# Kernel optimization log

Hardware: AMD Instinct MI355X
Metric: run time of the kernel (lower is better)

The kernel has to match this reference:

```python
import jax, jax.numpy as jnp
import numpy as np

H = W = 128          # render resolution
TS = 4               # texture_size from the module
DIST, ELEV, AZIM = 2.732, 0.0, 90.0   # camera (azimuth fixed for determinism)
BIG = 1e10


def setup_inputs() -> dict:
    key = jax.random.key(0)
    # UV-sphere mesh (stands in for nr.load_obj)
    nlat, nlon = 33, 40
    theta = np.linspace(0.15, np.pi - 0.15, nlat)
    phi = np.linspace(0.0, 2.0 * np.pi, nlon, endpoint=False)
    tt, pp = np.meshgrid(theta, phi, indexing='ij')
    verts = np.stack([np.sin(tt) * np.cos(pp), np.cos(tt), np.sin(tt) * np.sin(pp)], -1)
    verts = verts.reshape(-1, 3).astype(np.float32)          # [V,3]
    idx = lambda i, j: i * nlon + (j % nlon)
    faces = []
    for i in range(nlat - 1):
        for j in range(nlon):
            faces.append([idx(i, j), idx(i + 1, j), idx(i, j + 1)])
            faces.append([idx(i, j + 1), idx(i + 1, j), idx(i + 1, j + 1)])
    faces = np.asarray(faces, np.int32)                       # [F,3], F=2560
    k1, k2 = jax.random.split(key)
    textures = 0.1 * jax.random.normal(k1, (1, faces.shape[0], TS, TS, TS, 3), jnp.float32)
    image_ref = jax.random.uniform(k2, (1, 3, H, W), jnp.float32)
    return {
        'vertices': jnp.asarray(verts)[None],                 # [1,V,3]
        'textures': textures,                                 # [1,F,4,4,4,3]
        'image_ref': image_ref,                               # [1,3,H,W]
        'faces': jnp.asarray(faces)[None],                    # [1,F,3] int32
    }


def _look_at(v, eye):
    # neural_renderer look_at: at=origin, up=+y
    up = jnp.array([0.0, 1.0, 0.0], v.dtype)
    z = -eye / jnp.linalg.norm(eye)
    x = jnp.cross(up, z); x = x / jnp.linalg.norm(x)
    y = jnp.cross(z, x)
    R = jnp.stack([x, y, z])                                  # rows: camera axes
    return (v - eye) @ R.T


def _edge(a, b, p):
    # signed area cross product; a,b: [...,2], p broadcastable [...,2]
    return (b[..., 0] - a[..., 0]) * (p[..., 1] - a[..., 1]) - \
           (b[..., 1] - a[..., 1]) * (p[..., 0] - a[..., 0])


def reference(vertices, textures, image_ref, faces):
    el, az = jnp.deg2rad(ELEV), jnp.deg2rad(AZIM)
    eye = DIST * jnp.array([jnp.cos(el) * jnp.sin(az), jnp.sin(el), -jnp.cos(el) * jnp.cos(az)])

    v = _look_at(vertices[0], eye)                            # [V,3] camera space
    tri = v[faces[0]]                                         # [F,3,3]
    p2 = tri[..., :2]                                         # orthographic proj [F,3,2]
    z3 = tri[..., 2]                                          # [F,3]

    xs = (jnp.arange(W, dtype=jnp.float32) + 0.5) / W * 2.0 - 1.0
    ys = 1.0 - (jnp.arange(H, dtype=jnp.float32) + 0.5) / H * 2.0
    gy, gx = jnp.meshgrid(ys, xs, indexing='ij')
    px = jnp.stack([gx.ravel(), gy.ravel()], -1)              # [P,2]
    P = px.shape[0]

    a, b, c = p2[:, 0], p2[:, 1], p2[:, 2]                    # [F,2]
    area = _edge(a, b, c)                                     # [F]
    sa = jnp.where(jnp.abs(area) < 1e-8, 1e-8, area)
    pb = px[:, None, :]                                       # [P,1,2]
    w0 = _edge(b, c, pb) / sa                                 # [P,F]
    w1 = _edge(c, a, pb) / sa
    w2 = _edge(a, b, pb) / sa
    inside = (w0 >= 0) & (w1 >= 0) & (w2 >= 0) & (jnp.abs(area) >= 1e-8)
    depth = w0 * z3[:, 0] + w1 * z3[:, 1] + w2 * z3[:, 2]     # [P,F]
    zbuf = jnp.where(inside, depth, BIG)
    fidx = jnp.argmin(zbuf, axis=1)                           # [P] winning face
    hit = jnp.min(zbuf, axis=1) < BIG * 0.5                   # [P]

    # recompute barycentric only for the winning face (grads flow here)
    tw = p2[fidx]                                             # [P,3,2]
    zw = z3[fidx]                                             # [P,3]
    aw, bw, cw = tw[:, 0], tw[:, 1], tw[:, 2]
    arw = _edge(aw, bw, cw)
    srw = jnp.where(jnp.abs(arw) < 1e-8, 1e-8, arw)
    u0 = _edge(bw, cw, px) / srw
    u1 = _edge(cw, aw, px) / srw
    u2 = _edge(aw, bw, px) / srw
    w = jnp.clip(jnp.stack([u0, u1, u2], -1), 0.0, 1.0)       # [P,3]
    w = w / (jnp.sum(w, -1, keepdims=True) + 1e-8)

    # trilinear sample from per-face texture cube (ambient=1, directional=0)
    tex = jnp.tanh(textures)[0]                               # [F,TS,TS,TS,3]
    texf = tex[fidx]                                          # [P,TS,TS,TS,3]
    pos = w * (TS - 1)                                        # [P,3]
    lo = jnp.clip(jnp.floor(pos).astype(jnp.int32), 0, TS - 2)
    fr = pos - lo.astype(pos.dtype)                           # [P,3]
    pid = jnp.arange(P)
    col = jnp.zeros((P, 3), tex.dtype)
    for di in (0, 1):
        for dj in (0, 1):
            for dk in (0, 1):
                wgt = (fr[:, 0] if di else 1.0 - fr[:, 0]) * \
                      (fr[:, 1] if dj else 1.0 - fr[:, 1]) * \
                      (fr[:, 2] if dk else 1.0 - fr[:, 2])
                corner = texf[pid, lo[:, 0] + di, lo[:, 1] + dj, lo[:, 2] + dk]
                col = col + wgt[:, None] * corner

    flat = jnp.where(hit[:, None], col, 0.0)                  # [P,3]
    image = flat.reshape(H, W, 3).transpose(2, 0, 1)[None]    # [1,3,H,W]
    loss = jnp.sum((image - image_ref) ** 2)
    return loss
```

## Files before the change

kernel.cpp:

```cpp
#include <hip/hip_runtime.h>
#include <cmath>

#define H_ 128
#define W_ 128
#define P_ (H_ * W_)
#define NTX 16
#define NTY 16
#define NTILES (NTX * NTY)
#define CAP 512

struct Cam {
    float ex, ey, ez;
    float r00, r01, r02, r10, r11, r12, r20, r21, r22;
};

__global__ __launch_bounds__(512) void render_all(
    const float* __restrict__ verts, const int* __restrict__ faces, int F,
    Cam cam, const float* __restrict__ tex, const float* __restrict__ ref,
    double* __restrict__ partials) {
#pragma clang fp contract(off)
    __shared__ int lcnt;
    __shared__ int lfi[CAP];
    __shared__ float4 lrec[CAP * 3];
    __shared__ unsigned long long lbest[8 * 64];
    int t = blockIdx.x;
    int tid = threadIdx.x;
    int mytx = t & (NTX - 1), myty = t >> 4;
    if (tid == 0) lcnt = 0;
    __syncthreads();

    for (int f = tid; f < F; f += 512) {
        float tx[3], ty[3], tz[3];
        for (int k = 0; k < 3; ++k) {
            int vi = faces[f * 3 + k];
            float vx = verts[vi * 3 + 0];
            float vy = verts[vi * 3 + 1];
            float vz = verts[vi * 3 + 2];
            float dx = vx - cam.ex, dy = vy - cam.ey, dz = vz - cam.ez;
            tx[k] = (dx * cam.r00 + dy * cam.r01) + dz * cam.r02;
            ty[k] = (dx * cam.r10 + dy * cam.r11) + dz * cam.r12;
            tz[k] = (dx * cam.r20 + dy * cam.r21) + dz * cam.r22;
        }
        float a0 = tx[0], a1 = ty[0], b0 = tx[1], b1 = ty[1];
        float c0 = tx[2], c1 = ty[2];
        float area = (b0 - a0) * (c1 - a1) - (b1 - a1) * (c0 - a0);
        float ab = fabsf(area);
        if (ab < 1e-8f) continue;
        float sa = area;
        float minx = fminf(fminf(a0, b0), c0), maxx = fmaxf(fmaxf(a0, b0), c0);
        float miny = fminf(fminf(a1, b1), c1), maxy = fmaxf(fmaxf(a1, b1), c1);
        int colmin = (int)ceilf((minx + 1.0f) * 64.0f - 0.5f) - 1;
        int colmax = (int)floorf((maxx + 1.0f) * 64.0f - 0.5f) + 1;
        int rowmin = (int)ceilf((1.0f - maxy) * 64.0f - 0.5f) - 1;
        int rowmax = (int)floorf((1.0f - miny) * 64.0f - 0.5f) + 1;
        colmin = max(colmin, 0); colmax = min(colmax, W_ - 1);
        rowmin = max(rowmin, 0); rowmax = min(rowmax, H_ - 1);
        if (colmin > colmax || rowmin > rowmax) continue;
        if (mytx < (colmin >> 3) || mytx > (colmax >> 3) ||
            myty < (rowmin >> 3) || myty > (rowmax >> 3)) continue;
        int slot = atomicAdd(&lcnt, 1);
        if (slot < CAP) {
            lfi[slot] = f;
            lrec[slot * 3 + 0] = make_float4(a0, a1, b0, b1);
            lrec[slot * 3 + 1] = make_float4(c0, c1, tz[0], tz[1]);
            lrec[slot * 3 + 2] = make_float4(tz[2], sa, 0.0f, 0.0f);
        }
    }
    __syncthreads();
    int n = min(lcnt, CAP);

    int wv = tid >> 6, lane = tid & 63;
    int lx = lane & 7, ly = lane >> 3;
    int col = mytx * 8 + lx, row = myty * 8 + ly;
    int pid = row * W_ + col;
    float px = ((col + 0.5f) / 128.0f) * 2.0f - 1.0f;
    float py = 1.0f - ((row + 0.5f) / 128.0f) * 2.0f;
    unsigned long long best = ~0ull;
    for (int i = wv; i < n; i += 8) {
        float4 r0 = lrec[i * 3 + 0];
        float4 r1 = lrec[i * 3 + 1];
        float4 r2 = lrec[i * 3 + 2];
        float a0 = r0.x, a1 = r0.y, b0 = r0.z, b1 = r0.w;
        float c0 = r1.x, c1 = r1.y, z0 = r1.z, z1 = r1.w;
        float z2 = r2.x, sa = r2.y;
        float w0n = (c0 - b0) * (py - b1) - (c1 - b1) * (px - b0);
        float w1n = (a0 - c0) * (py - c1) - (a1 - c1) * (px - c0);
        float w2n = (b0 - a0) * (py - a1) - (b1 - a1) * (px - a0);
        bool ins;
        if (sa > 0.0f) ins = (w0n >= 0.0f) & (w1n >= 0.0f) & (w2n >= 0.0f);
        else           ins = (w0n <= 0.0f) & (w1n <= 0.0f) & (w2n <= 0.0f);
        if (ins) {
            float w0 = w0n / sa, w1 = w1n / sa, w2 = w2n / sa;
            float d = (w0 * z0 + w1 * z1) + w2 * z2;
            unsigned long long key =
                ((unsigned long long)__float_as_uint(d) << 32)
                | (unsigned)lfi[i];
            best = min(best, key);
        }
    }
    lbest[wv * 64 + lane] = best;
    __syncthreads();
    if (wv != 0) return;

    unsigned long long key = best;
    for (int s = 1; s < 8; ++s) key = min(key, lbest[s * 64 + lane]);
    float bd = __uint_as_float((unsigned)(key >> 32));
    bool hit = bd < 5e9f;
    int bestf = hit ? (int)(unsigned)(key & 0xffffffffu) : 0;
    float a0, a1, b0, b1, c0, c1, sa;
    {
        float tx[3], ty[3];
        for (int k = 0; k < 3; ++k) {
            int vi = faces[bestf * 3 + k];
            float vx = verts[vi * 3 + 0];
            float vy = verts[vi * 3 + 1];
            float vz = verts[vi * 3 + 2];
            float dx = vx - cam.ex, dy = vy - cam.ey, dz = vz - cam.ez;
            tx[k] = (dx * cam.r00 + dy * cam.r01) + dz * cam.r02;
            ty[k] = (dx * cam.r10 + dy * cam.r11) + dz * cam.r12;
        }
        a0 = tx[0]; a1 = ty[0]; b0 = tx[1]; b1 = ty[1]; c0 = tx[2]; c1 = ty[2];
        float area = (b0 - a0) * (c1 - a1) - (b1 - a1) * (c0 - a0);
        sa = (fabsf(area) < 1e-8f) ? 1e-8f : area;
    }
    float u0 = ((c0 - b0) * (py - b1) - (c1 - b1) * (px - b0)) / sa;
    float u1 = ((a0 - c0) * (py - c1) - (a1 - c1) * (px - c0)) / sa;
    float u2 = ((b0 - a0) * (py - a1) - (b1 - a1) * (px - a0)) / sa;
    float w0 = fminf(fmaxf(u0, 0.0f), 1.0f);
    float w1 = fminf(fmaxf(u1, 0.0f), 1.0f);
    float w2 = fminf(fmaxf(u2, 0.0f), 1.0f);
    float ssum = ((w0 + w1) + w2) + 1e-8f;
    float n0 = w0 / ssum, n1 = w1 / ssum, n2 = w2 / ssum;
    float p0 = n0 * 3.0f, p1 = n1 * 3.0f, p2 = n2 * 3.0f;
    int l0 = (int)floorf(p0); l0 = min(max(l0, 0), 2);
    int l1 = (int)floorf(p1); l1 = min(max(l1, 0), 2);
    int l2 = (int)floorf(p2); l2 = min(max(l2, 0), 2);
    float fr0 = p0 - (float)l0;
    float fr1 = p1 - (float)l1;
    float fr2 = p2 - (float)l2;
    const float* tb = tex + (size_t)bestf * 192;
    float cr = 0.0f, cg = 0.0f, cb = 0.0f;
    for (int di = 0; di < 2; ++di)
        for (int dj = 0; dj < 2; ++dj)
            for (int dk = 0; dk < 2; ++dk) {
                float wx = di ? fr0 : (1.0f - fr0);
                float wy = dj ? fr1 : (1.0f - fr1);
                float wz = dk ? fr2 : (1.0f - fr2);
                float wgt = (wx * wy) * wz;
                int off = (((l0 + di) * 4 + (l1 + dj)) * 4 + (l2 + dk)) * 3;
                cr = cr + wgt * tanhf(tb[off + 0]);
                cg = cg + wgt * tanhf(tb[off + 1]);
                cb = cb + wgt * tanhf(tb[off + 2]);
            }
    double acc = 0.0;
    {
        float fc = hit ? cr : 0.0f;
        float d = fc - ref[0 * P_ + pid];
        acc += (double)(d * d);
        fc = hit ? cg : 0.0f;
        d = fc - ref[1 * P_ + pid];
        acc += (double)(d * d);
        fc = hit ? cb : 0.0f;
        d = fc - ref[2 * P_ + pid];
        acc += (double)(d * d);
    }
    for (int off = 32; off > 0; off >>= 1) acc += __shfl_down(acc, off);
    if (lane == 0) partials[t] = acc;
}

__global__ __launch_bounds__(64) void finalize(
    const double* __restrict__ partials, float* __restrict__ out) {
    double v = 0.0;
    for (int k = 0; k < 4; ++k) v += partials[threadIdx.x * 4 + k];
    for (int off = 32; off > 0; off >>= 1) v += __shfl_xor(v, off);
    if (threadIdx.x == 0) out[0] = (float)v;
}

extern "C" void kernel_launch(void* const* d_in, const int* in_sizes, int n_in,
                              void* d_out, int out_size, void* d_ws, size_t ws_size,
                              hipStream_t stream) {
    const float* vertices = (const float*)d_in[0];
    const float* textures = (const float*)d_in[1];
    const float* image_ref = (const float*)d_in[2];
    const int* faces = (const int*)d_in[3];
    int F = in_sizes[3] / 3;

    float az = (float)(90.0 * M_PI / 180.0);
    float el = 0.0f;
    float ce = cosf(el), se = sinf(el);
    float sz = sinf(az), cz = cosf(az);
    const float DIST = 2.732f;
    float ex = DIST * (ce * sz);
    float ey = DIST * se;
    float ez = DIST * (-(ce * cz));
    float nrm = sqrtf((ex * ex + ey * ey) + ez * ez);
    float z0 = -ex / nrm, z1 = -ey / nrm, z2 = -ez / nrm;
    float x0 = 1.0f * z2 - 0.0f * z1;
    float x1 = 0.0f * z0 - 0.0f * z2;
    float x2 = 0.0f * z1 - 1.0f * z0;
    float xn = sqrtf((x0 * x0 + x1 * x1) + x2 * x2);
    x0 /= xn; x1 /= xn; x2 /= xn;
    float y0 = z1 * x2 - z2 * x1;
    float y1 = z2 * x0 - z0 * x2;
    float y2 = z0 * x1 - z1 * x0;
    Cam cam{ex, ey, ez, x0, x1, x2, y0, y1, y2, z0, z1, z2};

    double* partials = (double*)d_ws;

    hipLaunchKernelGGL(render_all, dim3(NTILES), dim3(512), 0, stream,
                       vertices, faces, F, cam, textures, image_ref, partials);
    hipLaunchKernelGGL(finalize, dim3(1), dim3(64), 0, stream,
                       partials, (float*)d_out);
}
```

Before: 18.16 us.

## Cache transformed vertices in LDS and fuse finalize into render kernel via flags

Each block now transforms all vertices once into shared memory and reads them from there during face binning and shading, instead of re-transforming three vertices per face from global memory. The separate finalize launch is removed. An extra block spin-waits on per-tile flags written with atomics and a fence, then reduces the partials and resets the flags. This saves a kernel launch and redundant vertex math, but depends on the extra block being co-resident with the others, adds spin-wait traffic, and assumes V fits in VMAX.

```diff
diff --git a/kernel.cpp b/kernel.cpp
--- a/kernel.cpp
+++ b/kernel.cpp
@@ -8,6 +8,8 @@
 #define NTY 16
 #define NTILES (NTX * NTY)
 #define CAP 512
+#define VMAX 1344
+#define MAGIC 0x5AFE5AFEu
 
 struct Cam {
     float ex, ey, ez;
@@ -15,38 +17,57 @@
 };
 
 __global__ __launch_bounds__(512) void render_all(
-    const float* __restrict__ verts, const int* __restrict__ faces, int F,
-    Cam cam, const float* __restrict__ tex, const float* __restrict__ ref,
-    double* __restrict__ partials) {
+    const float* __restrict__ verts, const int* __restrict__ faces,
+    int F, int V, Cam cam, const float* __restrict__ tex,
+    const float* __restrict__ ref, unsigned long long* __restrict__ partials,
+    unsigned int* __restrict__ flags, float* __restrict__ out) {
 #pragma clang fp contract(off)
+    int t = blockIdx.x;
+    int tid = threadIdx.x;
+
+    if (t == NTILES) {
+        if (tid >= 64) return;
+        double v = 0.0;
+        for (int k = 0; k < 4; ++k) {
+            int i = tid * 4 + k;
+            while (atomicAdd(&flags[i], 0u) != MAGIC)
+                __builtin_amdgcn_s_sleep(2);
+            unsigned long long bits = atomicAdd(&partials[i], 0ull);
+            v += __longlong_as_double((long long)bits);
+        }
+        for (int off = 32; off > 0; off >>= 1) v += __shfl_xor(v, off);
+        if (tid == 0) out[0] = (float)v;
+        for (int k = 0; k < 4; ++k)
+            atomicExch(&flags[tid * 4 + k], 0u);
+        return;
+    }
+
     __shared__ int lcnt;
+    __shared__ float lvx[VMAX], lvy[VMAX], lvz[VMAX];
     __shared__ int lfi[CAP];
     __shared__ float4 lrec[CAP * 3];
     __shared__ unsigned long long lbest[8 * 64];
-    int t = blockIdx.x;
-    int tid = threadIdx.x;
     int mytx = t & (NTX - 1), myty = t >> 4;
     if (tid == 0) lcnt = 0;
+    for (int v = tid; v < V; v += 512) {
+        float vx = verts[v * 3 + 0];
+        float vy = verts[v * 3 + 1];
+        float vz = verts[v * 3 + 2];
+        float dx = vx - cam.ex, dy = vy - cam.ey, dz = vz - cam.ez;
+        lvx[v] = (dx * cam.r00 + dy * cam.r01) + dz * cam.r02;
+        lvy[v] = (dx * cam.r10 + dy * cam.r11) + dz * cam.r12;
+        lvz[v] = (dx * cam.r20 + dy * cam.r21) + dz * cam.r22;
+    }
     __syncthreads();
 
     for (int f = tid; f < F; f += 512) {
-        float tx[3], ty[3], tz[3];
-        for (int k = 0; k < 3; ++k) {
-            int vi = faces[f * 3 + k];
-            float vx = verts[vi * 3 + 0];
-            float vy = verts[vi * 3 + 1];
-            float vz = verts[vi * 3 + 2];
-            float dx = vx - cam.ex, dy = vy - cam.ey, dz = vz - cam.ez;
-            tx[k] = (dx * cam.r00 + dy * cam.r01) + dz * cam.r02;
-            ty[k] = (dx * cam.r10 + dy * cam.r11) + dz * cam.r12;
-            tz[k] = (dx * cam.r20 + dy * cam.r21) + dz * cam.r22;
-        }
-        float a0 = tx[0], a1 = ty[0], b0 = tx[1], b1 = ty[1];
-        float c0 = tx[2], c1 = ty[2];
+        int i0 = faces[f * 3 + 0], i1 = faces[f * 3 + 1], i2 = faces[f * 3 + 2];
+        float a0 = lvx[i0], a1 = lvy[i0];
+        float b0 = lvx[i1], b1 = lvy[i1];
+        float c0 = lvx[i2], c1 = lvy[i2];
         float area = (b0 - a0) * (c1 - a1) - (b1 - a1) * (c0 - a0);
         float ab = fabsf(area);
         if (ab < 1e-8f) continue;
-        float sa = area;
         float minx = fminf(fminf(a0, b0), c0), maxx = fmaxf(fmaxf(a0, b0), c0);
         float miny = fminf(fminf(a1, b1), c1), maxy = fmaxf(fmaxf(a1, b1), c1);
         int colmin = (int)ceilf((minx + 1.0f) * 64.0f - 0.5f) - 1;
@@ -62,8 +83,8 @@
         if (slot < CAP) {
             lfi[slot] = f;
             lrec[slot * 3 + 0] = make_float4(a0, a1, b0, b1);
-            lrec[slot * 3 + 1] = make_float4(c0, c1, tz[0], tz[1]);
-            lrec[slot * 3 + 2] = make_float4(tz[2], sa, 0.0f, 0.0f);
+            lrec[slot * 3 + 1] = make_float4(c0, c1, lvz[i0], lvz[i1]);
+            lrec[slot * 3 + 2] = make_float4(lvz[i2], area, 0.0f, 0.0f);
         }
     }
     __syncthreads();
@@ -107,22 +128,13 @@
     float bd = __uint_as_float((unsigned)(key >> 32));
     bool hit = bd < 5e9f;
     int bestf = hit ? (int)(unsigned)(key & 0xffffffffu) : 0;
-    float a0, a1, b0, b1, c0, c1, sa;
-    {
-        float tx[3], ty[3];
-        for (int k = 0; k < 3; ++k) {
-            int vi = faces[bestf * 3 + k];
-            float vx = verts[vi * 3 + 0];
-            float vy = verts[vi * 3 + 1];
-            float vz = verts[vi * 3 + 2];
-            float dx = vx - cam.ex, dy = vy - cam.ey, dz = vz - cam.ez;
-            tx[k] = (dx * cam.r00 + dy * cam.r01) + dz * cam.r02;
-            ty[k] = (dx * cam.r10 + dy * cam.r11) + dz * cam.r12;
-        }
-        a0 = tx[0]; a1 = ty[0]; b0 = tx[1]; b1 = ty[1]; c0 = tx[2]; c1 = ty[2];
-        float area = (b0 - a0) * (c1 - a1) - (b1 - a1) * (c0 - a0);
-        sa = (fabsf(area) < 1e-8f) ? 1e-8f : area;
-    }
+    int i0 = faces[bestf * 3 + 0], i1 = faces[bestf * 3 + 1],
+        i2 = faces[bestf * 3 + 2];
+    float a0 = lvx[i0], a1 = lvy[i0];
+    float b0 = lvx[i1], b1 = lvy[i1];
+    float c0 = lvx[i2], c1 = lvy[i2];
+    float area = (b0 - a0) * (c1 - a1) - (b1 - a1) * (c0 - a0);
+    float sa = (fabsf(area) < 1e-8f) ? 1e-8f : area;
     float u0 = ((c0 - b0) * (py - b1) - (c1 - b1) * (px - b0)) / sa;
     float u1 = ((a0 - c0) * (py - c1) - (a1 - c1) * (px - c0)) / sa;
     float u2 = ((b0 - a0) * (py - a1) - (b1 - a1) * (px - a0)) / sa;
@@ -165,15 +177,12 @@
         acc += (double)(d * d);
     }
     for (int off = 32; off > 0; off >>= 1) acc += __shfl_down(acc, off);
-    if (lane == 0) partials[t] = acc;
-}
-
-__global__ __launch_bounds__(64) void finalize(
-    const double* __restrict__ partials, float* __restrict__ out) {
-    double v = 0.0;
-    for (int k = 0; k < 4; ++k) v += partials[threadIdx.x * 4 + k];
-    for (int off = 32; off > 0; off >>= 1) v += __shfl_xor(v, off);
-    if (threadIdx.x == 0) out[0] = (float)v;
+    if (lane == 0) {
+        atomicExch(&partials[t],
+                   (unsigned long long)__double_as_longlong(acc));
+        __threadfence();
+        atomicExch(&flags[t], MAGIC);
+    }
 }
 
 extern "C" void kernel_launch(void* const* d_in, const int* in_sizes, int n_in,
@@ -183,6 +192,7 @@
     const float* textures = (const float*)d_in[1];
     const float* image_ref = (const float*)d_in[2];
     const int* faces = (const int*)d_in[3];
+    int V = in_sizes[0] / 3;
     int F = in_sizes[3] / 3;
 
     float az = (float)(90.0 * M_PI / 180.0);
@@ -205,10 +215,10 @@
     float y2 = z0 * x1 - z1 * x0;
     Cam cam{ex, ey, ez, x0, x1, x2, y0, y1, y2, z0, z1, z2};
 
-    double* partials = (double*)d_ws;
-
-    hipLaunchKernelGGL(render_all, dim3(NTILES), dim3(512), 0, stream,
-                       vertices, faces, F, cam, textures, image_ref, partials);
-    hipLaunchKernelGGL(finalize, dim3(1), dim3(64), 0, stream,
-                       partials, (float*)d_out);
+    unsigned long long* partials = (unsigned long long*)d_ws;
+    unsigned int* flags = (unsigned int*)((char*)d_ws + 256 * 8);
+
+    hipLaunchKernelGGL(render_all, dim3(NTILES + 1), dim3(512), 0, stream,
+                       vertices, faces, F, V, cam, textures, image_ref,
+                       partials, flags, (float*)d_out);
 }
```

New measurement: 19.33 us. 1.06x slower.
